# Kernel optimization log

Hardware: AMD Instinct MI355X
Metric: run time of the kernel (lower is better)

Reference implementation:

```python
import jax, jax.numpy as jnp
import numpy as np

B, F, DEPTH = 8192, 256, 6

def entmax15(x):
    # exact 1.5-entmax along the last axis (sort-based algorithm)
    x = x / 2.0
    x = x - jnp.max(x, axis=-1, keepdims=True)
    xs = -jnp.sort(-x, axis=-1)                      # descending sort
    d = x.shape[-1]
    rho = jnp.arange(1, d + 1, dtype=x.dtype)
    mean = jnp.cumsum(xs, axis=-1) / rho
    mean_sq = jnp.cumsum(xs * xs, axis=-1) / rho
    ss = rho * (mean_sq - mean * mean)
    tau = mean - jnp.sqrt(jnp.clip((1.0 - ss) / rho, 0.0))
    support = jnp.sum((tau <= xs).astype(jnp.int32), axis=-1)
    tau_star = jnp.take_along_axis(tau, (support - 1)[..., None], axis=-1)
    return jnp.square(jnp.clip(x - tau_star, 0.0))

def _stump_level(x_in, fm, cp, lr):
    # x_in: [B,Fd]; fm: [n,Fd]; cp,lr: [n,Fd,2]. Vectorized over all n stumps of a level.
    mask = entmax15(fm)                                      # [n,Fd] feature gating
    w = jnp.array([1.0, 2.0], dtype=x_in.dtype)              # cutpoint-bin weights W
    z = entmax15(x_in[None, :, :, None] * w - cp[:, None])   # [n,B,Fd,2] binning
    out = jnp.einsum('nbfl,nfl,nf->nbl', z, lr, mask)        # leaf responses, masked sum over features
    # torch.cat of per-stump [B,2] along dim=1 -> [B, n*2]
    return jnp.transpose(out, (1, 0, 2)).reshape(x_in.shape[0], -1), mask

def _forward(x, params):
    tree_input = x
    masks = []
    out = None
    for fm, cp, lr in params:
        out, m = _stump_level(tree_input, fm, cp, lr)
        tree_input = jnp.concatenate([x, out], axis=1)
        masks.append(m)
    return out, masks

def setup_inputs() -> dict:
    key = jax.random.key(0)
    ks = jax.random.split(key, 1 + 3 * DEPTH)
    inp = {"x": jax.random.normal(ks[0], (B, F), dtype=jnp.float32)}
    for d in range(DEPTH):
        n = 2 ** d
        Fd = F + (2 ** d if d > 0 else 0)
        inp[f"fm{d}"] = jax.random.uniform(ks[1 + 3 * d], (n, Fd), dtype=jnp.float32)
        inp[f"cp{d}"] = jax.random.uniform(ks[2 + 3 * d], (n, Fd, 2), dtype=jnp.float32)
        inp[f"lr{d}"] = jax.random.uniform(ks[3 + 3 * d], (n, Fd, 2), dtype=jnp.float32)
    return inp

def reference(x, fm0, cp0, lr0, fm1, cp1, lr1, fm2, cp2, lr2, fm3, cp3, lr3, fm4, cp4, lr4, fm5, cp5, lr5):
    params = [(fm0, cp0, lr0), (fm1, cp1, lr1), (fm2, cp2, lr2),
              (fm3, cp3, lr3), (fm4, cp4, lr4), (fm5, cp5, lr5)]
    out, masks = _forward(x, params)  # dropout=0 -> identity
    return (out, *masks)
```

## Files before the change

kernel.cpp:

```cpp
#include <hip/hip_runtime.h>

#define B_SZ 8192
#define XST 17


struct MaskArgs {
  const float* fm[6];
  const float* cp[6];
  const float* lr[6];
  float* out_masks;
  float4* cprm;
  int* cnt;
  float* cstf;
};

__device__ __forceinline__ float wave_max(float v) {
#pragma unroll
  for (int o = 32; o > 0; o >>= 1) v = fmaxf(v, __shfl_xor(v, o));
  return v;
}
__device__ __forceinline__ float wave_sum(float v) {
#pragma unroll
  for (int o = 32; o > 0; o >>= 1) v += __shfl_xor(v, o);
  return v;
}

__global__ __launch_bounds__(64) void ndt_masks(MaskArgs a) {
  const int maskOff[6] = {524288, 524544, 525060, 526100, 528212, 532564};
  const int prmOff[6]  = {0, 256, 772, 1812, 3924, 8276};
  const int cstOff[6]  = {0, 1, 3, 7, 15, 31};
  const int exBase[6]  = {0, 256, 258, 262, 270, 286};
  int bid = blockIdx.x, lane = threadIdx.x;
  int d = 0, s = bid, n = 1;
  while (s >= n) { s -= n; n <<= 1; ++d; }
  int Fd = 256 + ((d > 0) ? n : 0);

  const float* fm = a.fm[d] + (size_t)s * Fd;
  float y[5];
#pragma unroll
  for (int j = 0; j < 5; ++j) {
    int f = lane + 64 * j;
    y[j] = (f < Fd) ? fm[f] * 0.5f : -3.0e38f;
  }
  float m = fmaxf(fmaxf(fmaxf(y[0], y[1]), fmaxf(y[2], y[3])), y[4]);
  m = wave_max(m);
#pragma unroll
  for (int j = 0; j < 5; ++j) y[j] -= m;

  float lo = -1.f, hi = 0.f;
  for (int it = 0; it < 24; ++it) {
    float tau = 0.5f * (lo + hi);
    float ss = 0.f;
#pragma unroll
    for (int j = 0; j < 5; ++j) {
      float v = fmaxf(y[j] - tau, 0.f);
      ss = __builtin_fmaf(v, v, ss);
    }
    ss = wave_sum(ss);
    if (ss >= 1.f) lo = tau; else hi = tau;
  }
  float tau = 0.5f * (lo + hi);

  float* mo = a.out_masks + maskOff[d] + (size_t)s * Fd;
  const float* cp = a.cp[d] + (size_t)s * Fd * 2;
  const float* lr = a.lr[d] + (size_t)s * Fd * 2;
  float4* cpr = a.cprm + prmOff[d] + (size_t)s * Fd;
  int exB = exBase[d];
  float sum0 = 0.f, sum1 = 0.f;
  int base = 0;
#pragma unroll
  for (int j = 0; j < 5; ++j) {
    int f = lane + 64 * j;
    bool in = (f < Fd);
    float v = fmaxf(y[j] - tau, 0.f);
    float mk = v * v;
    float c10 = 0.f, ml0 = 0.f, ml1 = 0.f;
    if (in) {
      mo[f] = mk;
      float c0 = cp[2 * f], c1 = cp[2 * f + 1];
      ml0 = lr[2 * f] * mk;
      ml1 = lr[2 * f + 1] * mk;
      c10 = c1 - c0;
      sum0 += ml0;
      sum1 += ml1;
    }
    bool act = in && (v > 0.f);
    unsigned long long bm = __ballot(act);
    int pre = __popcll(bm & ((1ull << lane) - 1ull));
    if (act) {
      int fidx = (f < 256) ? f : (exB + f - 256);
      cpr[base + pre] =
          make_float4(c10, ml0 * 0.125f, ml1 * 0.125f, __int_as_float(fidx));
    }
    base += __popcll(bm);
  }
  sum0 = wave_sum(sum0);
  sum1 = wave_sum(sum1);
  if (lane == 0) {
    a.cstf[2 * (cstOff[d] + s)] = 0.5f * sum0;
    a.cstf[2 * (cstOff[d] + s) + 1] = 0.5f * sum1;
    a.cnt[cstOff[d] + s] = base;
  }
}

__device__ __forceinline__ float entpair(float c10, float xv) {
  float t = c10 - xv;
  float tc = __builtin_amdgcn_fmed3f(t, -2.f, 2.f);
  float u = __builtin_fmaf(tc, -tc, 8.0f);
  return tc * __builtin_amdgcn_sqrtf(u);
}

template <int N, int FD>
__device__ __forceinline__ void ndt_level(const float4* __restrict__ cp,
                                          const int* __restrict__ cN,
                                          const float* __restrict__ cs,
                                          int outRow, int g, int l,
                                          float* __restrict__ pbuf,
                                          float* __restrict__ xls) {
  constexpr int SPG = 64 / N;
  int s = g / SPG, slice = g - s * SPG;
  int nc = cN[s];
  const float4* ps = cp + (size_t)s * FD;
  float a00 = 0.f, a10 = 0.f, a01 = 0.f, a11 = 0.f;
  int jlo = slice * nc / SPG, jhi = (slice + 1) * nc / SPG;
#pragma unroll 4
  for (int j = jlo; j < jhi; ++j) {
    float4 p = ps[j];
    int row = __float_as_int(p.w);
    float xv0 = xls[row * XST + l];
    float xv1 = xls[row * XST + l + 8];
    float e0 = entpair(p.x, xv0);
    float e1 = entpair(p.x, xv1);
    a00 = __builtin_fmaf(e0, p.y, a00);
    a10 = __builtin_fmaf(-e0, p.z, a10);
    a01 = __builtin_fmaf(e1, p.y, a01);
    a11 = __builtin_fmaf(-e1, p.z, a11);
  }
  pbuf[g * 32 + l] = a00;
  pbuf[g * 32 + l + 8] = a01;
  pbuf[g * 32 + 16 + l] = a10;
  pbuf[g * 32 + 16 + l + 8] = a11;
  __syncthreads();
  int tid = g * 8 + l;
  for (int t = tid; t < 2 * N * 16; t += 512) {
    int o = t >> 4, cc = t & 15;
    int s2 = o >> 1, par = o & 1;
    float v = cs[o];
#pragma unroll
    for (int k = 0; k < SPG; ++k)
      v += pbuf[(s2 * SPG + k) * 32 + par * 16 + cc];
    xls[(outRow + o) * XST + cc] = v;
  }
  __syncthreads();
}

__global__ __launch_bounds__(512, 4) void ndt_all(const float* __restrict__ x,
                                                  const float4* __restrict__ cprm,
                                                  const int* __restrict__ cnt,
                                                  const float* __restrict__ cstf,
                                                  float* __restrict__ out) {
  __shared__ float xls[382 * XST];
  __shared__ float pbuf[64 * 32];
  int tid = threadIdx.x;
  int g = tid >> 3, l = tid & 7;
  int b0 = blockIdx.x * 16;
  {
    int c = tid >> 5, seg = tid & 31;
    const float* xp = x + (size_t)(b0 + c) * 256 + seg;
#pragma unroll
    for (int j = 0; j < 8; ++j) xls[(seg + 32 * j) * XST + c] = xp[32 * j];
  }
  __syncthreads();
  ndt_level<1, 256>(cprm, cnt, cstf, 256, g, l, pbuf, xls);
  ndt_level<2, 258>(cprm + 256, cnt + 1, cstf + 2, 258, g, l, pbuf, xls);
  ndt_level<4, 260>(cprm + 772, cnt + 3, cstf + 6, 262, g, l, pbuf, xls);
  ndt_level<8, 264>(cprm + 1812, cnt + 7, cstf + 14, 270, g, l, pbuf, xls);
  ndt_level<16, 272>(cprm + 3924, cnt + 15, cstf + 30, 286, g, l, pbuf, xls);
  ndt_level<32, 288>(cprm + 8276, cnt + 31, cstf + 62, 318, g, l, pbuf, xls);
  {
    int c = tid >> 5, oo = (tid & 31) * 2;
    float2 v = make_float2(xls[(318 + oo) * XST + c], xls[(319 + oo) * XST + c]);
    *(float2*)(out + (size_t)(b0 + c) * 64 + oo) = v;
  }
}

extern "C" void kernel_launch(void* const* d_in, const int* in_sizes, int n_in,
                              void* d_out, int out_size, void* d_ws, size_t ws_size,
                              hipStream_t stream) {
  const float* x = (const float*)d_in[0];
  float* out = (float*)d_out;
  float* wsf = (float*)d_ws;

  float4* cprm = (float4*)(wsf + 2575872);
  float* cstf = wsf + 2645840;
  int* cnt = (int*)(wsf + 2645966);

  MaskArgs ma;
  for (int d = 0; d < 6; ++d) {
    ma.fm[d] = (const float*)d_in[1 + 3 * d];
    ma.cp[d] = (const float*)d_in[2 + 3 * d];
    ma.lr[d] = (const float*)d_in[3 + 3 * d];
  }
  ma.out_masks = out;
  ma.cprm = cprm;
  ma.cnt = cnt;
  ma.cstf = cstf;
  hipLaunchKernelGGL(ndt_masks, dim3(63), dim3(64), 0, stream, ma);

  hipLaunchKernelGGL(ndt_all, dim3(B_SZ / 16), dim3(512), 0, stream,
                     x, cprm, cnt, cstf, out);
}
```

Baseline: 37.65 us.

## Process 32 rows per 1024-thread block and reduce partials with wave shuffles

Each block now covers 32 batch rows with 1024 threads, and each thread accumulates 4 rows per cutpoint parameter. Each float4 parameter load is therefore reused across more rows. The cross-slice reduction of partial sums now runs through __shfl_xor inside a wave, and the shared-memory partial buffer plus its extra pass are only used when a stump spans several waves. This cuts LDS traffic and barrier work per row, but raises per-thread register use and halves the number of blocks, which may reduce occupancy.

```diff
diff --git a/kernel.cpp b/kernel.cpp
--- a/kernel.cpp
+++ b/kernel.cpp
@@ -1,7 +1,7 @@
 #include <hip/hip_runtime.h>
 
 #define B_SZ 8192
-#define XST 17
+#define XST 33
 
 
 struct MaskArgs {
@@ -114,56 +114,96 @@
 __device__ __forceinline__ void ndt_level(const float4* __restrict__ cp,
                                           const int* __restrict__ cN,
                                           const float* __restrict__ cs,
-                                          int outRow, int g, int l,
-                                          float* __restrict__ pbuf,
-                                          float* __restrict__ xls) {
-  constexpr int SPG = 64 / N;
+                                          int outRow, int tid,
+                                          float* __restrict__ xls,
+                                          float* __restrict__ pbuf) {
+  constexpr int SPG = 128 / N;
+  int g = tid >> 3, l = tid & 7;
   int s = g / SPG, slice = g - s * SPG;
   int nc = cN[s];
   const float4* ps = cp + (size_t)s * FD;
-  float a00 = 0.f, a10 = 0.f, a01 = 0.f, a11 = 0.f;
+  float a0[4], a1[4];
+#pragma unroll
+  for (int k = 0; k < 4; ++k) {
+    a0[k] = 0.f;
+    a1[k] = 0.f;
+  }
   int jlo = slice * nc / SPG, jhi = (slice + 1) * nc / SPG;
 #pragma unroll 4
   for (int j = jlo; j < jhi; ++j) {
     float4 p = ps[j];
     int row = __float_as_int(p.w);
-    float xv0 = xls[row * XST + l];
-    float xv1 = xls[row * XST + l + 8];
-    float e0 = entpair(p.x, xv0);
-    float e1 = entpair(p.x, xv1);
-    a00 = __builtin_fmaf(e0, p.y, a00);
-    a10 = __builtin_fmaf(-e0, p.z, a10);
-    a01 = __builtin_fmaf(e1, p.y, a01);
-    a11 = __builtin_fmaf(-e1, p.z, a11);
-  }
-  pbuf[g * 32 + l] = a00;
-  pbuf[g * 32 + l + 8] = a01;
-  pbuf[g * 32 + 16 + l] = a10;
-  pbuf[g * 32 + 16 + l + 8] = a11;
-  __syncthreads();
-  int tid = g * 8 + l;
-  for (int t = tid; t < 2 * N * 16; t += 512) {
-    int o = t >> 4, cc = t & 15;
-    int s2 = o >> 1, par = o & 1;
-    float v = cs[o];
-#pragma unroll
-    for (int k = 0; k < SPG; ++k)
-      v += pbuf[(s2 * SPG + k) * 32 + par * 16 + cc];
-    xls[(outRow + o) * XST + cc] = v;
-  }
-  __syncthreads();
-}
-
-__global__ __launch_bounds__(512, 4) void ndt_all(const float* __restrict__ x,
-                                                  const float4* __restrict__ cprm,
-                                                  const int* __restrict__ cnt,
-                                                  const float* __restrict__ cstf,
-                                                  float* __restrict__ out) {
+    int rb = row * XST + l;
+#pragma unroll
+    for (int k = 0; k < 4; ++k) {
+      float xv = xls[rb + 8 * k];
+      float e = entpair(p.x, xv);
+      a0[k] = __builtin_fmaf(e, p.y, a0[k]);
+      a1[k] = __builtin_fmaf(-e, p.z, a1[k]);
+    }
+  }
+  if (SPG <= 8) {
+#pragma unroll
+    for (int m = SPG / 2; m >= 1; m >>= 1) {
+#pragma unroll
+      for (int k = 0; k < 4; ++k) {
+        a0[k] += __shfl_xor(a0[k], 8 * m);
+        a1[k] += __shfl_xor(a1[k], 8 * m);
+      }
+    }
+    if (slice == 0) {
+      int R = outRow + 2 * s;
+      float c0 = cs[2 * s];
+#pragma unroll
+      for (int k = 0; k < 4; ++k) xls[R * XST + l + 8 * k] = a0[k] + c0;
+    } else if (slice == 1) {
+      int R = outRow + 2 * s + 1;
+      float c1 = cs[2 * s + 1];
+#pragma unroll
+      for (int k = 0; k < 4; ++k) xls[R * XST + l + 8 * k] = a1[k] + c1;
+    }
+    __syncthreads();
+  } else {
+#pragma unroll
+    for (int m = 4; m >= 1; m >>= 1) {
+#pragma unroll
+      for (int k = 0; k < 4; ++k) {
+        a0[k] += __shfl_xor(a0[k], 8 * m);
+        a1[k] += __shfl_xor(a1[k], 8 * m);
+      }
+    }
+    int w = tid >> 6, lw = tid & 63;
+    if (lw < 8) {
+#pragma unroll
+      for (int k = 0; k < 4; ++k) pbuf[w * 64 + l + 8 * k] = a0[k];
+    } else if (lw < 16) {
+#pragma unroll
+      for (int k = 0; k < 4; ++k) pbuf[w * 64 + 32 + l + 8 * k] = a1[k];
+    }
+    __syncthreads();
+    constexpr int WPS = SPG / 8;
+    if (tid < 2 * N * 32) {
+      int o = tid >> 5, cc = tid & 31;
+      int s2 = o >> 1, par = o & 1;
+      float v = cs[o];
+#pragma unroll
+      for (int k = 0; k < WPS; ++k)
+        v += pbuf[(s2 * WPS + k) * 64 + par * 32 + cc];
+      xls[(outRow + o) * XST + cc] = v;
+    }
+    __syncthreads();
+  }
+}
+
+__global__ __launch_bounds__(1024, 4) void ndt_all(const float* __restrict__ x,
+                                                   const float4* __restrict__ cprm,
+                                                   const int* __restrict__ cnt,
+                                                   const float* __restrict__ cstf,
+                                                   float* __restrict__ out) {
   __shared__ float xls[382 * XST];
-  __shared__ float pbuf[64 * 32];
+  __shared__ float pbuf[16 * 64];
   int tid = threadIdx.x;
-  int g = tid >> 3, l = tid & 7;
-  int b0 = blockIdx.x * 16;
+  int b0 = blockIdx.x * 32;
   {
     int c = tid >> 5, seg = tid & 31;
     const float* xp = x + (size_t)(b0 + c) * 256 + seg;
@@ -171,12 +211,12 @@
     for (int j = 0; j < 8; ++j) xls[(seg + 32 * j) * XST + c] = xp[32 * j];
   }
   __syncthreads();
-  ndt_level<1, 256>(cprm, cnt, cstf, 256, g, l, pbuf, xls);
-  ndt_level<2, 258>(cprm + 256, cnt + 1, cstf + 2, 258, g, l, pbuf, xls);
-  ndt_level<4, 260>(cprm + 772, cnt + 3, cstf + 6, 262, g, l, pbuf, xls);
-  ndt_level<8, 264>(cprm + 1812, cnt + 7, cstf + 14, 270, g, l, pbuf, xls);
-  ndt_level<16, 272>(cprm + 3924, cnt + 15, cstf + 30, 286, g, l, pbuf, xls);
-  ndt_level<32, 288>(cprm + 8276, cnt + 31, cstf + 62, 318, g, l, pbuf, xls);
+  ndt_level<1, 256>(cprm, cnt, cstf, 256, tid, xls, pbuf);
+  ndt_level<2, 258>(cprm + 256, cnt + 1, cstf + 2, 258, tid, xls, pbuf);
+  ndt_level<4, 260>(cprm + 772, cnt + 3, cstf + 6, 262, tid, xls, pbuf);
+  ndt_level<8, 264>(cprm + 1812, cnt + 7, cstf + 14, 270, tid, xls, pbuf);
+  ndt_level<16, 272>(cprm + 3924, cnt + 15, cstf + 30, 286, tid, xls, pbuf);
+  ndt_level<32, 288>(cprm + 8276, cnt + 31, cstf + 62, 318, tid, xls, pbuf);
   {
     int c = tid >> 5, oo = (tid & 31) * 2;
     float2 v = make_float2(xls[(318 + oo) * XST + c], xls[(319 + oo) * XST + c]);
@@ -207,6 +247,6 @@
   ma.cstf = cstf;
   hipLaunchKernelGGL(ndt_masks, dim3(63), dim3(64), 0, stream, ma);
 
-  hipLaunchKernelGGL(ndt_all, dim3(B_SZ / 16), dim3(512), 0, stream,
+  hipLaunchKernelGGL(ndt_all, dim3(B_SZ / 32), dim3(1024), 0, stream,
                      x, cprm, cnt, cstf, out);
 }
```

Measured after the change: 38.29 us. Within noise of the previous version (+1.7%).
